# Optimization experiments

Hardware: AMD Instinct MI355X
Metric: run time of the kernel (lower is better)

The kernel has to match this reference:

```python
import jax, jax.numpy as jnp
import numpy as np

HIDDEN = 128
IN_DIM = 15
NUM_REL = 4
N_NODES = 100000
N_EDGES = 2000000
N_GRAPHS = 64


def setup_inputs() -> dict:
    key = jax.random.key(0)
    ks = jax.random.split(key, 10)
    x = jax.random.normal(ks[0], (N_NODES, IN_DIM), dtype=jnp.float32)
    edge_index = jax.random.randint(ks[1], (2, N_EDGES), 0, N_NODES, dtype=jnp.int64)
    edge_type = jax.random.randint(ks[2], (N_EDGES,), 0, NUM_REL, dtype=jnp.int64)
    batch = jnp.sort(jax.random.randint(ks[3], (N_NODES,), 0, N_GRAPHS, dtype=jnp.int64))
    s1 = 1.0 / np.sqrt(IN_DIM)
    s2 = 1.0 / np.sqrt(HIDDEN)
    W1 = jax.random.uniform(ks[4], (NUM_REL, IN_DIM, HIDDEN), jnp.float32, -s1, s1)
    root1 = jax.random.uniform(ks[5], (IN_DIM, HIDDEN), jnp.float32, -s1, s1)
    b1 = jnp.zeros((HIDDEN,), jnp.float32)
    W2 = jax.random.uniform(ks[6], (NUM_REL, HIDDEN, HIDDEN), jnp.float32, -s2, s2)
    root2 = jax.random.uniform(ks[7], (HIDDEN, HIDDEN), jnp.float32, -s2, s2)
    b2 = jnp.zeros((HIDDEN,), jnp.float32)
    return {"x": x, "W1": W1, "root1": root1, "b1": b1,
            "W2": W2, "root2": root2, "b2": b2,
            "edge_index": edge_index, "edge_type": edge_type, "batch": batch}


def _rgcn_conv(x, edge_index, edge_type, W, root, bias):
    # PyG RGCNConv: out = x @ root + bias + sum_r mean_{edges of rel r}(x_src) @ W_r
    src, dst = edge_index[0], edge_index[1]
    x_src = x[src]                                   # [E, d] gather
    out = x @ root + bias                            # [N, H]
    for r in range(NUM_REL):
        mask = (edge_type == r).astype(x.dtype)      # [E]
        agg = jax.ops.segment_sum(x_src * mask[:, None], dst, num_segments=x.shape[0])
        cnt = jax.ops.segment_sum(mask, dst, num_segments=x.shape[0])
        mean = agg / jnp.maximum(cnt, 1.0)[:, None]  # mean aggr; 0 for isolated nodes
        out = out + mean @ W[r]
    return out


def reference(x, W1, root1, b1, W2, root2, b2, edge_index, edge_type, batch):
    h = jax.nn.relu(_rgcn_conv(x, edge_index, edge_type, W1, root1, b1))
    h = jax.nn.relu(_rgcn_conv(h, edge_index, edge_type, W2, root2, b2))
    # global_mean_pool over graphs
    sums = jax.ops.segment_sum(h, batch, num_segments=N_GRAPHS)
    cnts = jax.ops.segment_sum(jnp.ones((h.shape[0],), h.dtype), batch, num_segments=N_GRAPHS)
    return sums / jnp.maximum(cnts, 1.0)[:, None]
```

## Files before the change

kernel.cpp:

```cpp
#include <hip/hip_runtime.h>
#include <hip/hip_fp16.h>

#define HIDDEN   128
#define IN_DIM   15
#define NUM_REL  4
#define N_NODES  100000
#define N_EDGES  2000000
#define N_GRAPHS 64

#define CAPR 32
#define CAP  (NUM_REL*CAPR)
#define G1 8
#define G2 16
#define KTOT 640
#define APAD 648

typedef _Float16 f16x8 __attribute__((ext_vector_type(8)));
typedef float    f32x4 __attribute__((ext_vector_type(4)));

__device__ __forceinline__ void fadd(float* p, float v) {
    unsafeAtomicAdd(p, v);
}

__global__ void build_csr(const int* __restrict__ ei, const int* __restrict__ et,
                          int* __restrict__ c4, int* __restrict__ sorted) {
    int e = blockIdx.x * blockDim.x + threadIdx.x;
    if (e >= N_EDGES) return;
    int s = ei[e];
    int d = ei[N_EDGES + e];
    int r = et[e];
    int slot = atomicAdd(&c4[d * NUM_REL + r], 1);
    if (slot < CAPR)
        sorted[(size_t)d * CAP + r * CAPR + slot] = s;
}

__global__ void w2conv(const float* __restrict__ W2, const float* __restrict__ root2,
                       __half* __restrict__ W2s) {
    int idx = blockIdx.x * blockDim.x + threadIdx.x;
    if (idx >= KTOT * HIDDEN) return;
    int k = idx >> 7, n = idx & 127;
    float v = (k < NUM_REL * HIDDEN) ? W2[k * HIDDEN + n]
                                     : root2[(k - NUM_REL * HIDDEN) * HIDDEN + n];
    int kk = k >> 5, krem = k & 31, hi = krem >> 3, ii = krem & 7;
    int ct = n >> 4, lo = n & 15;
    int lane = hi * 16 + lo;
    W2s[((((size_t)kk * 8 + ct) * 64 + lane) << 3) + ii] = __float2half(v);
}

__global__ __launch_bounds__(64) void agg1_kernel(
    const int* __restrict__ sorted, const int* __restrict__ c4,
    const float* __restrict__ x, float* __restrict__ agg1) {
    int n = blockIdx.x;
    int t = threadIdx.x;
    int r = t >> 4, col = t & 15;
    if (col >= IN_DIM) return;
    int deg = min(c4[n * NUM_REL + r], CAPR);
    const int* lst = sorted + (size_t)n * CAP + r * CAPR;
    float acc = 0.f;
    for (int e = 0; e < deg; ++e)
        acc += x[(size_t)lst[e] * IN_DIM + col];
    agg1[(size_t)n * (NUM_REL * IN_DIM) + r * IN_DIM + col] = acc;
}

__global__ __launch_bounds__(128) void node_pass1(
    const float* __restrict__ x, const int* __restrict__ c4,
    const float* __restrict__ agg1, const float* __restrict__ root1,
    const float* __restrict__ b1, const float* __restrict__ W1,
    __half* __restrict__ h16) {
    __shared__ float sxm[G1][76];
    int n0 = blockIdx.x * G1;
    int t  = threadIdx.x;

    for (int i = t; i < G1 * 75; i += 128) {
        int g = i / 75, k = i % 75;
        int n = n0 + g;
        float v = 0.f;
        if (k < IN_DIM) {
            v = x[(size_t)n * IN_DIM + k];
        } else {
            int rj = k - IN_DIM;
            int r  = rj / IN_DIM;
            float c = (float)c4[n * NUM_REL + r];
            v = agg1[(size_t)n * (NUM_REL * IN_DIM) + rj] / fmaxf(c, 1.f);
        }
        sxm[g][k] = v;
    }
    __syncthreads();

    int dcol = t;
    float acc[G1];
#pragma unroll
    for (int g = 0; g < G1; ++g) acc[g] = b1[dcol];
#pragma unroll
    for (int j = 0; j < IN_DIM; ++j) {
        float w = root1[j * HIDDEN + dcol];
#pragma unroll
        for (int g = 0; g < G1; ++g) acc[g] += sxm[g][j] * w;
    }
    for (int rj = 0; rj < NUM_REL * IN_DIM; ++rj) {
        float w = W1[rj * HIDDEN + dcol];
#pragma unroll
        for (int g = 0; g < G1; ++g) acc[g] += sxm[g][IN_DIM + rj] * w;
    }
#pragma unroll
    for (int g = 0; g < G1; ++g)
        h16[(size_t)(n0 + g) * HIDDEN + dcol] = __float2half(fmaxf(acc[g], 0.f));
}

__global__ __launch_bounds__(256) void layer2_kernel(
    const int* __restrict__ sorted, const int* __restrict__ c4,
    const __half* __restrict__ h16, const __half* __restrict__ W2s,
    const float* __restrict__ b2, const int* __restrict__ batch,
    float* __restrict__ out) {
    __shared__ __half A[G2][APAD];
    int n0 = blockIdx.x * G2;
    int t  = threadIdx.x;

    {
        int q    = t & 31;
        int r    = (t >> 5) & 3;
        int gsub = t >> 7;
        for (int gg = 0; gg < G2 / 2; ++gg) {
            int g = gg * 2 + gsub;
            int n = n0 + g;
            int c = c4[n * NUM_REL + r];
            int d = min(c, CAPR);
            const int* lst = sorted + (size_t)n * CAP + r * CAPR;
            float ax = 0.f, ay = 0.f, az = 0.f, aw = 0.f;
            float bx = 0.f, by = 0.f, bz = 0.f, bw = 0.f;
            int e = 0;
            for (; e + 2 <= d; e += 2) {
                uint2 u0 = *reinterpret_cast<const uint2*>(
                    h16 + (size_t)lst[e]     * HIDDEN + 4 * q);
                uint2 u1 = *reinterpret_cast<const uint2*>(
                    h16 + (size_t)lst[e + 1] * HIDDEN + 4 * q);
                float2 f0 = __half22float2(*reinterpret_cast<__half2*>(&u0.x));
                float2 f1 = __half22float2(*reinterpret_cast<__half2*>(&u0.y));
                float2 f2 = __half22float2(*reinterpret_cast<__half2*>(&u1.x));
                float2 f3 = __half22float2(*reinterpret_cast<__half2*>(&u1.y));
                ax += f0.x; ay += f0.y; az += f1.x; aw += f1.y;
                bx += f2.x; by += f2.y; bz += f3.x; bw += f3.y;
            }
            if (e < d) {
                uint2 u0 = *reinterpret_cast<const uint2*>(
                    h16 + (size_t)lst[e] * HIDDEN + 4 * q);
                float2 f0 = __half22float2(*reinterpret_cast<__half2*>(&u0.x));
                float2 f1 = __half22float2(*reinterpret_cast<__half2*>(&u0.y));
                ax += f0.x; ay += f0.y; az += f1.x; aw += f1.y;
            }
            float inv = 1.f / (float)max(c, 1);
            __half2* dst = reinterpret_cast<__half2*>(&A[g][r * HIDDEN + 4 * q]);
            dst[0] = __floats2half2_rn((ax + bx) * inv, (ay + by) * inv);
            dst[1] = __floats2half2_rn((az + bz) * inv, (aw + bw) * inv);
        }
        int col = t & 127, gs = t >> 7;
        for (int gg = 0; gg < G2 / 2; ++gg) {
            int g = gg * 2 + gs;
            A[g][4 * HIDDEN + col] = h16[(size_t)(n0 + g) * HIDDEN + col];
        }
    }
    __syncthreads();

    int lane = t & 63, w = t >> 6;
    int ln15 = lane & 15, khi = lane >> 4;
    f32x4 acc[2];
#pragma unroll
    for (int j = 0; j < 2; ++j) {
        float bb = b2[(w * 2 + j) * 16 + ln15];
        acc[j] = (f32x4){bb, bb, bb, bb};
    }
    for (int kk = 0; kk < KTOT / 32; ++kk) {
        f16x8 af = *reinterpret_cast<const f16x8*>(&A[ln15][kk * 32 + khi * 8]);
#pragma unroll
        for (int j = 0; j < 2; ++j) {
            f16x8 bf = *reinterpret_cast<const f16x8*>(
                W2s + ((((size_t)kk * 8 + w * 2 + j) * 64 + lane) << 3));
            acc[j] = __builtin_amdgcn_mfma_f32_16x16x32_f16(af, bf, acc[j], 0, 0, 0);
        }
    }

    bool uni = (batch[n0] == batch[n0 + G2 - 1]);
    int gb0 = batch[n0];
#pragma unroll
    for (int j = 0; j < 2; ++j) {
        int ct = w * 2 + j;
        int col = ct * 16 + ln15;
        if (uni) {
            float v = fmaxf(acc[j][0], 0.f) + fmaxf(acc[j][1], 0.f)
                    + fmaxf(acc[j][2], 0.f) + fmaxf(acc[j][3], 0.f);
            v += __shfl_xor(v, 16);
            v += __shfl_xor(v, 32);
            if (lane < 16) fadd(&out[gb0 * HIDDEN + ct * 16 + lane], v);
        } else {
#pragma unroll
            for (int reg = 0; reg < 4; ++reg) {
                int n = n0 + khi * 4 + reg;
                fadd(&out[batch[n] * HIDDEN + col], fmaxf(acc[j][reg], 0.f));
            }
        }
    }
}

__global__ void gcnt_kernel(const int* __restrict__ batch, float* __restrict__ gcnt) {
    int g = blockIdx.x * blockDim.x + threadIdx.x;
    if (g >= N_GRAPHS) return;
    int lo = 0, hi = N_NODES;
    while (lo < hi) { int m = (lo + hi) >> 1; if (batch[m] < g) lo = m + 1; else hi = m; }
    int begin = lo;
    lo = 0; hi = N_NODES;
    while (lo < hi) { int m = (lo + hi) >> 1; if (batch[m] < g + 1) lo = m + 1; else hi = m; }
    gcnt[g] = (float)(lo - begin);
}

__global__ void div_kernel(float* __restrict__ out, const float* __restrict__ gcnt) {
    int i = blockIdx.x * blockDim.x + threadIdx.x;
    if (i < N_GRAPHS * HIDDEN) out[i] /= fmaxf(gcnt[i / HIDDEN], 1.f);
}

extern "C" void kernel_launch(void* const* d_in, const int* in_sizes, int n_in,
                              void* d_out, int out_size, void* d_ws, size_t ws_size,
                              hipStream_t stream) {
    const float* x     = (const float*)d_in[0];
    const float* W1    = (const float*)d_in[1];
    const float* root1 = (const float*)d_in[2];
    const float* b1    = (const float*)d_in[3];
    const float* W2    = (const float*)d_in[4];
    const float* root2 = (const float*)d_in[5];
    const float* b2    = (const float*)d_in[6];
    const int*   ei    = (const int*)d_in[7];
    const int*   et    = (const int*)d_in[8];
    const int*   batch = (const int*)d_in[9];
    float* out = (float*)d_out;

    int*    c4     = (int*)d_ws;
    int*    sorted = c4 + 400000;
    float*  agg1   = (float*)(sorted + (size_t)N_NODES * CAP);
    __half* h16    = (__half*)(agg1 + 6000000);
    __half* W2s    = h16 + 12800000;
    float*  gcnt   = (float*)(W2s + 81920);

    hipMemsetAsync(c4, 0, (size_t)400000 * sizeof(int), stream);
    hipMemsetAsync(out, 0, (size_t)N_GRAPHS * HIDDEN * sizeof(float), stream);

    build_csr<<<(N_EDGES + 255) / 256, 256, 0, stream>>>(ei, et, c4, sorted);
    w2conv<<<(KTOT * HIDDEN + 255) / 256, 256, 0, stream>>>(W2, root2, W2s);
    agg1_kernel<<<N_NODES, 64, 0, stream>>>(sorted, c4, x, agg1);
    node_pass1<<<N_NODES / G1, 128, 0, stream>>>(x, c4, agg1, root1, b1, W1, h16);
    layer2_kernel<<<N_NODES / G2, 256, 0, stream>>>(sorted, c4, h16, W2s, b2,
                                                    batch, out);
    gcnt_kernel<<<1, 64, 0, stream>>>(batch, gcnt);
    div_kernel<<<(N_GRAPHS * HIDDEN + 255) / 256, 256, 0, stream>>>(out, gcnt);
}
```

Before: 509.5 us.

## Replace direct atomic CSR build with bucketed histogram, scan, scatter and local placement

The single edge-binning kernel, which did random global atomics and scattered writes into the per-node slot array, is replaced by a four-stage pipeline. A histogram counts edges per 64-node bucket, a single-block scan computes bucket offsets, a scatter packs each edge (source, relation, local destination) into a bucket-contiguous staging buffer, and a per-bucket block places edges into slots using shared-memory atomics. The aim is to make the final slot writes local to a bucket and to move the slot-claiming atomics into shared memory. The cost is two extra passes over the edge list, a staging buffer and three more kernel launches, and slot order within a destination becomes nondeterministic in a different way.

```diff
diff --git a/kernel.cpp b/kernel.cpp
--- a/kernel.cpp
+++ b/kernel.cpp
@@ -10,6 +10,8 @@
 
 #define CAPR 32
 #define CAP  (NUM_REL*CAPR)
+#define BSH  6
+#define NBUCK ((N_NODES + 63) >> BSH)
 #define G1 8
 #define G2 16
 #define KTOT 640
@@ -22,16 +24,68 @@
     unsafeAtomicAdd(p, v);
 }
 
-__global__ void build_csr(const int* __restrict__ ei, const int* __restrict__ et,
-                          int* __restrict__ c4, int* __restrict__ sorted) {
+__global__ void hist_kernel(const int* __restrict__ ei, const int* __restrict__ et,
+                            int* __restrict__ c4, int* __restrict__ bhist) {
+    int e = blockIdx.x * blockDim.x + threadIdx.x;
+    if (e >= N_EDGES) return;
+    int d = ei[N_EDGES + e];
+    int r = et[e];
+    atomicAdd(&c4[d * NUM_REL + r], 1);
+    atomicAdd(&bhist[d >> BSH], 1);
+}
+
+__global__ __launch_bounds__(1024) void scan_kernel(
+    const int* __restrict__ bhist, int* __restrict__ boffs, int* __restrict__ bcur) {
+    __shared__ int sh[2048];
+    int t = threadIdx.x;
+    for (int i = t; i < 2048; i += 1024) sh[i] = (i < NBUCK) ? bhist[i] : 0;
+    __syncthreads();
+    for (int off = 1; off < 2048; off <<= 1) {
+        int i0 = t, i1 = t + 1024;
+        int v0 = (i0 >= off) ? sh[i0 - off] : 0;
+        int v1 = (i1 >= off) ? sh[i1 - off] : 0;
+        __syncthreads();
+        sh[i0] += v0; sh[i1] += v1;
+        __syncthreads();
+    }
+    for (int i = t; i < NBUCK; i += 1024) {
+        int v = (i == 0) ? 0 : sh[i - 1];
+        boffs[i] = v; bcur[i] = v;
+    }
+    if (t == 0) boffs[NBUCK] = sh[NBUCK - 1];
+}
+
+__global__ void scatter_kernel(const int* __restrict__ ei, const int* __restrict__ et,
+                               int* __restrict__ bcur, int* __restrict__ staging) {
     int e = blockIdx.x * blockDim.x + threadIdx.x;
     if (e >= N_EDGES) return;
     int s = ei[e];
     int d = ei[N_EDGES + e];
     int r = et[e];
-    int slot = atomicAdd(&c4[d * NUM_REL + r], 1);
-    if (slot < CAPR)
-        sorted[(size_t)d * CAP + r * CAPR + slot] = s;
+    int pos = atomicAdd(&bcur[d >> BSH], 1);
+    staging[pos] = s | (r << 17) | ((d & 63) << 19);
+}
+
+__global__ __launch_bounds__(256) void place_kernel(
+    const int* __restrict__ staging, const int* __restrict__ boffs,
+    int* __restrict__ sorted) {
+    __shared__ int cur[64 * NUM_REL];
+    int b = blockIdx.x;
+    int t = threadIdx.x;
+    for (int i = t; i < 64 * NUM_REL; i += 256) cur[i] = 0;
+    __syncthreads();
+    int base = boffs[b], end = boffs[b + 1];
+    for (int i = base + t; i < end; i += 256) {
+        int u = staging[i];
+        int s = u & 0x1FFFF;
+        int r = (u >> 17) & 3;
+        int dl = (u >> 19) & 63;
+        int slot = atomicAdd(&cur[dl * NUM_REL + r], 1);
+        if (slot < CAPR) {
+            int d = (b << BSH) + dl;
+            sorted[(size_t)d * CAP + r * CAPR + slot] = s;
+        }
+    }
 }
 
 __global__ void w2conv(const float* __restrict__ W2, const float* __restrict__ root2,
@@ -232,17 +286,24 @@
     const int*   batch = (const int*)d_in[9];
     float* out = (float*)d_out;
 
-    int*    c4     = (int*)d_ws;
-    int*    sorted = c4 + 400000;
-    float*  agg1   = (float*)(sorted + (size_t)N_NODES * CAP);
-    __half* h16    = (__half*)(agg1 + 6000000);
-    __half* W2s    = h16 + 12800000;
-    float*  gcnt   = (float*)(W2s + 81920);
-
-    hipMemsetAsync(c4, 0, (size_t)400000 * sizeof(int), stream);
+    int*    c4      = (int*)d_ws;
+    int*    bhist   = c4 + 400000;
+    int*    boffs   = bhist + NBUCK;
+    int*    bcur    = boffs + NBUCK + 1;
+    int*    staging = bcur + NBUCK;
+    int*    sorted  = staging + N_EDGES;
+    float*  agg1    = (float*)(sorted + (size_t)N_NODES * CAP);
+    __half* h16     = (__half*)(agg1 + 6000000);
+    __half* W2s     = h16 + 12800000;
+    float*  gcnt    = (float*)(W2s + 81920);
+
+    hipMemsetAsync(c4, 0, (size_t)(400000 + NBUCK) * sizeof(int), stream);
     hipMemsetAsync(out, 0, (size_t)N_GRAPHS * HIDDEN * sizeof(float), stream);
 
-    build_csr<<<(N_EDGES + 255) / 256, 256, 0, stream>>>(ei, et, c4, sorted);
+    hist_kernel<<<(N_EDGES + 255) / 256, 256, 0, stream>>>(ei, et, c4, bhist);
+    scan_kernel<<<1, 1024, 0, stream>>>(bhist, boffs, bcur);
+    scatter_kernel<<<(N_EDGES + 255) / 256, 256, 0, stream>>>(ei, et, bcur, staging);
+    place_kernel<<<NBUCK, 256, 0, stream>>>(staging, boffs, sorted);
     w2conv<<<(KTOT * HIDDEN + 255) / 256, 256, 0, stream>>>(W2, root2, W2s);
     agg1_kernel<<<N_NODES, 64, 0, stream>>>(sorted, c4, x, agg1);
     node_pass1<<<N_NODES / G1, 128, 0, stream>>>(x, c4, agg1, root1, b1, W1, h16);
```

Result: slower. 1.070 ms (+109.9%).
